# Optimization experiments

Hardware: AMD Instinct MI355X
Metric: run time of the kernel (lower is better)

## Reference

```python
import jax, jax.numpy as jnp
import numpy as np
import math

B, M, V, C, HID, BIN, H, W = 2, 1024, 300, 128, 128, 256, 384, 512


def fibonacci_sphere(n):
    # generate_grasp_views: n approximately-uniform directions on the unit sphere
    i = np.arange(n, dtype=np.float64)
    phi = (np.sqrt(5.0) - 1.0) / 2.0
    z = (2.0 * i + 1.0) / n - 1.0
    r = np.sqrt(np.maximum(1.0 - z * z, 0.0))
    t = 2.0 * np.pi * i * phi
    v = np.stack([r * np.cos(t), r * np.sin(t), z], -1)
    return (v / np.linalg.norm(v, axis=-1, keepdims=True)).astype(np.float32)


def setup_inputs():
    key = jax.random.key(0)
    ks = jax.random.split(key, 24)
    seed_features = jax.random.normal(ks[0], (B, C, M), jnp.float32)
    token_sel_idx = jax.random.randint(ks[1], (B, M), 0, H * W)
    fx = 525.0
    Kmat = jnp.array([[fx, 0.0, W / 2.0], [0.0, fx, H / 2.0], [0.0, 0.0, 1.0]], jnp.float32)
    K = jnp.broadcast_to(Kmat, (B, 3, 3))
    depth_map = 0.2 + 0.8 * jax.random.uniform(ks[2], (B, 1, H, W), jnp.float32)
    depth_prob = jax.nn.softmax(jax.random.normal(ks[3], (B, BIN, H, W), jnp.float32), axis=1)
    view_dirs = jnp.asarray(fibonacci_sphere(V))

    def lin(k, fan_in, shape):
        s = 1.0 / np.sqrt(fan_in)
        return jax.random.uniform(k, shape, jnp.float32, -s, s)

    qin = C + 7  # seed_feat + ray(3) + normal(3) + uncert(1)
    params = dict(
        Wq1=lin(ks[4], qin, (qin, HID)), bq1=lin(ks[5], qin, (HID,)),
        Wq2=lin(ks[6], HID, (HID, HID)), bq2=lin(ks[7], HID, (HID,)),
        Wa1=lin(ks[8], 3, (3, HID)), ba1=lin(ks[9], 3, (HID,)),
        Wa2=lin(ks[10], HID, (HID, HID)), ba2=lin(ks[11], HID, (HID,)),
        Wb1=lin(ks[12], 3, (3, HID // 2)), bb1=lin(ks[13], 3, (HID // 2,)),
        Wb2=lin(ks[14], HID // 2, (HID // 2, 1)), bb2=lin(ks[15], HID // 2, (1,)),
        Wr1=lin(ks[16], HID, (HID, C)), br1=lin(ks[17], HID, (C,)),
        Wr2=lin(ks[18], C, (C, C)), br2=lin(ks[19], C, (C,)),
    )
    return dict(seed_features=seed_features, token_sel_idx=token_sel_idx, K=K,
                depth_map=depth_map, depth_prob=depth_prob, view_dirs=view_dirs, **params)


def _views_to_rot(views):
    # batch_viewpoint_params_to_matrix(-views, angle=0)
    axis_x = -views
    zero = jnp.zeros_like(axis_x[..., 0])
    axis_y = jnp.stack([-axis_x[..., 1], axis_x[..., 0], zero], -1)
    ny = jnp.linalg.norm(axis_y, axis=-1, keepdims=True)
    fallback = jnp.broadcast_to(jnp.array([0.0, 1.0, 0.0], views.dtype), axis_y.shape)
    axis_y = jnp.where(ny < 1e-8, fallback, axis_y / jnp.maximum(ny, 1e-8))
    axis_x = axis_x / jnp.maximum(jnp.linalg.norm(axis_x, axis=-1, keepdims=True), 1e-8)
    axis_z = jnp.cross(axis_x, axis_y)
    return jnp.stack([axis_x, axis_y, axis_z], -1)  # (B,M,3,3)


def _forward(seed_features, token_sel_idx, K, depth_map, depth_prob, view_dirs,
             Wq1, bq1, Wq2, bq2, Wa1, ba1, Wa2, ba2, Wb1, bb1, Wb2, bb2, Wr1, br1, Wr2, br2):
    depth_map = jax.lax.stop_gradient(depth_map)   # .detach() in torch
    depth_prob = jax.lax.stop_gradient(depth_prob)
    # --- backproject depth to xyz map (B,3,H,W) ---
    ys, xs = jnp.meshgrid(jnp.arange(H, dtype=jnp.float32), jnp.arange(W, dtype=jnp.float32), indexing='ij')
    fx = K[:, 0, 0][:, None, None, None]; fy = K[:, 1, 1][:, None, None, None]
    cx = K[:, 0, 2][:, None, None, None]; cy = K[:, 1, 2][:, None, None, None]
    z = depth_map
    x = (xs[None, None] - cx) / fx * z
    y = (ys[None, None] - cy) / fy * z
    xyz = jnp.concatenate([x, y, z], axis=1)
    # --- central-difference normal map with replicate pad ---
    dx = (xyz[:, :, :, 2:] - xyz[:, :, :, :-2])[:, :, 1:-1, :]
    dy = (xyz[:, :, 2:, :] - xyz[:, :, :-2, :])[:, :, :, 1:-1]
    n = jnp.cross(dx.transpose(0, 2, 3, 1), dy.transpose(0, 2, 3, 1))
    n = n / jnp.maximum(jnp.linalg.norm(n, axis=-1, keepdims=True), 1e-6)
    normal_map = jnp.pad(n.transpose(0, 3, 1, 2), ((0, 0), (0, 0), (1, 1), (1, 1)), mode='edge')
    # --- depth uncertainty: normalized entropy over bins ---
    p = jnp.maximum(depth_prob, 1e-8)
    uncert_map = jnp.clip(-(p * jnp.log(p)).sum(axis=1, keepdims=True) / math.log(BIN), 0.0, 1.0)
    # --- per-seed irregular gathers ---
    def gather(feat, idx):
        Bf, Cf = feat.shape[0], feat.shape[1]
        flat = feat.reshape(Bf, Cf, H * W)
        return jnp.take_along_axis(flat, jnp.broadcast_to(idx[:, None, :], (Bf, Cf, idx.shape[1])), axis=2)
    normal_bm3 = gather(normal_map, token_sel_idx).transpose(0, 2, 1)  # (B,M,3)
    uncert_bm1 = gather(uncert_map, token_sel_idx).transpose(0, 2, 1)  # (B,M,1)
    u = (token_sel_idx % W).astype(jnp.float32)
    v = (token_sel_idx // W).astype(jnp.float32)
    rx = (u - K[:, 0, 2][:, None]) / K[:, 0, 0][:, None]
    ry = (v - K[:, 1, 2][:, None]) / K[:, 1, 1][:, None]
    rays = jnp.stack([rx, ry, jnp.ones_like(rx)], -1)
    rays = rays / jnp.maximum(jnp.linalg.norm(rays, axis=-1, keepdims=True), 1e-12)
    normal_bm3 = normal_bm3 * (1.0 - uncert_bm1)
    # --- query / anchor / bias MLPs ---
    q_in = jnp.concatenate([seed_features.transpose(0, 2, 1), rays, normal_bm3, uncert_bm1], -1)
    q = jax.nn.relu(jax.nn.relu(q_in @ Wq1 + bq1) @ Wq2 + bq2)          # (B,M,HID)
    a = jax.nn.relu(view_dirs @ Wa1 + ba1) @ Wa2 + ba2                  # (V,HID)
    bias = (jax.nn.relu(view_dirs @ Wb1 + bb1) @ Wb2 + bb2)[:, 0]        # (V,)
    logits = jnp.einsum('bmh,vh->bmv', q, a) / jnp.sqrt(jnp.float32(HID)) + bias
    view_score = jax.nn.sigmoid(logits)                                  # (B,M,V)
    # --- top-1 view selection + gather xyz / rot / anchor feat ---
    top_inds = jnp.argmax(view_score, axis=-1)                           # (B,M)
    top_xyz = view_dirs[top_inds]                                        # (B,M,3)
    rot = _views_to_rot(top_xyz)                                         # (B,M,3,3)
    top_a = a[top_inds]                                                  # (B,M,HID)
    res = jax.nn.relu((q + top_a) @ Wr1 + br1) @ Wr2 + br2               # (B,M,C)
    res_feat = res.transpose(0, 2, 1)                                    # (B,C,M)
    return view_score, top_inds, top_xyz, rot, res_feat


def reference(seed_features, token_sel_idx, K, depth_map, depth_prob, view_dirs,
              Wq1, bq1, Wq2, bq2, Wa1, ba1, Wa2, ba2, Wb1, bb1, Wb2, bb2, Wr1, br1, Wr2, br2):
    return _forward(seed_features, token_sel_idx, K, depth_map, depth_prob, view_dirs,
                    Wq1, bq1, Wq2, bq2, Wa1, ba1, Wa2, ba2, Wb1, bb1, Wb2, bb2, Wr1, br1, Wr2, br2)
```

## Files before the change

kernel.cpp:

```cpp
#include <hip/hip_runtime.h>
#include <math.h>

#define B 2
#define M 1024
#define V 300
#define C 128
#define HID 128
#define BIN 256
#define H 384
#define W 512
#define QIN (C + 7)
#define G 4

__global__ __launch_bounds__(HID) void anchor_kernel(
    const float* __restrict__ view_dirs,
    const float* __restrict__ Wa1, const float* __restrict__ ba1,
    const float* __restrict__ Wa2, const float* __restrict__ ba2,
    const float* __restrict__ Wb1, const float* __restrict__ bb1,
    const float* __restrict__ Wb2, const float* __restrict__ bb2,
    float* __restrict__ a_out, float* __restrict__ aT_out,
    float* __restrict__ bias_out) {
  const int v = blockIdx.x;
  const int t = threadIdx.x;
  __shared__ float h1[HID];

  const float vd0 = view_dirs[v * 3 + 0];
  const float vd1 = view_dirs[v * 3 + 1];
  const float vd2 = view_dirs[v * 3 + 2];

  float h = vd0 * Wa1[0 * HID + t] + vd1 * Wa1[1 * HID + t] + vd2 * Wa1[2 * HID + t] + ba1[t];
  h1[t] = fmaxf(h, 0.0f);

  if (t < 64) {
    float x = vd0 * Wb1[0 * 64 + t] + vd1 * Wb1[1 * 64 + t] + vd2 * Wb1[2 * 64 + t] + bb1[t];
    x = fmaxf(x, 0.0f) * Wb2[t];
#pragma unroll
    for (int o = 32; o > 0; o >>= 1) x += __shfl_down(x, o, 64);
    if (t == 0) bias_out[v] = x + bb2[0];
  }
  __syncthreads();

  float acc = ba2[t];
#pragma unroll 8
  for (int k = 0; k < HID; ++k) acc += h1[k] * Wa2[k * HID + t];
  a_out[v * HID + t] = acc;
  aT_out[(size_t)t * V + v] = acc;
}

__global__ __launch_bounds__(128) void seed_kernel(
    const float* __restrict__ seed, const int* __restrict__ token_sel_idx,
    const float* __restrict__ Kmat, const float* __restrict__ depth_map,
    const float* __restrict__ depth_prob, const float* __restrict__ view_dirs,
    const float* __restrict__ Wq1, const float* __restrict__ bq1,
    const float* __restrict__ Wq2, const float* __restrict__ bq2,
    const float* __restrict__ Wr1, const float* __restrict__ br1,
    const float* __restrict__ Wr2, const float* __restrict__ br2,
    const float* __restrict__ a_ws, const float* __restrict__ aT_ws,
    const float* __restrict__ bias_ws,
    float* __restrict__ out_view_score, float* __restrict__ out_top_inds,
    float* __restrict__ out_top_xyz, float* __restrict__ out_rot,
    float* __restrict__ out_res) {
  const int s0 = blockIdx.x * G;
  const int b = s0 >> 10;
  const int m0 = s0 & (M - 1);
  const int t = threadIdx.x;
  const int lane = t & 63;
  const int wv = t >> 6;

  __shared__ __align__(16) float qin_s[G][136];
  __shared__ __align__(16) float hs[G][HID];
  __shared__ __align__(16) float qs[G][HID];
  __shared__ __align__(16) float sum_s[G][HID];
  __shared__ float ered[G][2];
  __shared__ float wbv[G][2];
  __shared__ int   wbi[G][2];
  __shared__ int   sbest[G];
  __shared__ int   sidx[G];

  if (t < G) sidx[t] = token_sel_idx[b * M + m0 + t];

  {
    const float4 sv = *(const float4*)&seed[((size_t)b * C + t) * M + m0];
    qin_s[0][t] = sv.x; qin_s[1][t] = sv.y; qin_s[2][t] = sv.z; qin_s[3][t] = sv.w;
  }
  if (t < G) qin_s[t][135] = 0.0f;
  __syncthreads();

  {
    const size_t HW = (size_t)H * W;
    float e[G];
#pragma unroll
    for (int g = 0; g < G; ++g) {
      const float* dp = depth_prob + (size_t)b * BIN * HW + sidx[g];
      const float p0 = fmaxf(dp[(size_t)(2 * t + 0) * HW], 1e-8f);
      const float p1 = fmaxf(dp[(size_t)(2 * t + 1) * HW], 1e-8f);
      e[g] = p0 * logf(p0) + p1 * logf(p1);
    }
#pragma unroll
    for (int o = 32; o > 0; o >>= 1) {
#pragma unroll
      for (int g = 0; g < G; ++g) e[g] += __shfl_down(e[g], o, 64);
    }
    if (lane == 0) {
#pragma unroll
      for (int g = 0; g < G; ++g) ered[g][wv] = e[g];
    }
  }
  __syncthreads();

  if (t < G) {
    const int g = t;
    const int idx = sidx[g];
    float uncert = (-(ered[g][0] + ered[g][1])) / 5.5451774444795623f;
    uncert = fminf(fmaxf(uncert, 0.0f), 1.0f);

    const float fx = Kmat[b * 9 + 0], fy = Kmat[b * 9 + 4];
    const float cx = Kmat[b * 9 + 2], cy = Kmat[b * 9 + 5];
    const int w = idx % W;
    const int h = idx / W;
    const int hc = min(max(h, 1), H - 2);
    const int wc = min(max(w, 1), W - 2);

    const float* dm = depth_map + (size_t)b * H * W;
    const float zl = dm[hc * W + (wc - 1)];
    const float zr = dm[hc * W + (wc + 1)];
    const float zu = dm[(hc - 1) * W + wc];
    const float zd = dm[(hc + 1) * W + wc];

    const float dxx = (wc + 1 - cx) / fx * zr - (wc - 1 - cx) / fx * zl;
    const float dxy = (hc - cy) / fy * zr - (hc - cy) / fy * zl;
    const float dxz = zr - zl;
    const float dyx = (wc - cx) / fx * zd - (wc - cx) / fx * zu;
    const float dyy = (hc + 1 - cy) / fy * zd - (hc - 1 - cy) / fy * zu;
    const float dyz = zd - zu;

    float nx = dxy * dyz - dxz * dyy;
    float ny = dxz * dyx - dxx * dyz;
    float nz = dxx * dyy - dxy * dyx;
    const float nn = fmaxf(sqrtf(nx * nx + ny * ny + nz * nz), 1e-6f);
    const float sc = (1.0f - uncert) / nn;

    const float rx = ((float)w - cx) / fx;
    const float ry = ((float)h - cy) / fy;
    const float rn = fmaxf(sqrtf(rx * rx + ry * ry + 1.0f), 1e-12f);

    qin_s[g][128] = rx / rn;
    qin_s[g][129] = ry / rn;
    qin_s[g][130] = 1.0f / rn;
    qin_s[g][131] = nx * sc;
    qin_s[g][132] = ny * sc;
    qin_s[g][133] = nz * sc;
    qin_s[g][134] = uncert;
  }
  __syncthreads();

  {
    float acc[G];
    const float b1 = bq1[t];
#pragma unroll
    for (int g = 0; g < G; ++g) acc[g] = b1;
    for (int i0 = 0; i0 < 132; i0 += 4) {
      const float w0 = Wq1[(i0 + 0) * HID + t];
      const float w1 = Wq1[(i0 + 1) * HID + t];
      const float w2 = Wq1[(i0 + 2) * HID + t];
      const float w3 = Wq1[(i0 + 3) * HID + t];
#pragma unroll
      for (int g = 0; g < G; ++g) {
        const float4 qv = *(const float4*)&qin_s[g][i0];
        acc[g] += qv.x * w0 + qv.y * w1 + qv.z * w2 + qv.w * w3;
      }
    }
    {
      const float w0 = Wq1[132 * HID + t];
      const float w1 = Wq1[133 * HID + t];
      const float w2 = Wq1[134 * HID + t];
#pragma unroll
      for (int g = 0; g < G; ++g) {
        const float4 qv = *(const float4*)&qin_s[g][132];
        acc[g] += qv.x * w0 + qv.y * w1 + qv.z * w2;
      }
    }
#pragma unroll
    for (int g = 0; g < G; ++g) hs[g][t] = fmaxf(acc[g], 0.0f);
  }
  __syncthreads();

  {
    float acc[G];
    const float b2 = bq2[t];
#pragma unroll
    for (int g = 0; g < G; ++g) acc[g] = b2;
    for (int k0 = 0; k0 < HID; k0 += 4) {
      const float w0 = Wq2[(k0 + 0) * HID + t];
      const float w1 = Wq2[(k0 + 1) * HID + t];
      const float w2 = Wq2[(k0 + 2) * HID + t];
      const float w3 = Wq2[(k0 + 3) * HID + t];
#pragma unroll
      for (int g = 0; g < G; ++g) {
        const float4 hv = *(const float4*)&hs[g][k0];
        acc[g] += hv.x * w0 + hv.y * w1 + hv.z * w2 + hv.w * w3;
      }
    }
#pragma unroll
    for (int g = 0; g < G; ++g) qs[g][t] = fmaxf(acc[g], 0.0f);
  }
  __syncthreads();

  const int col2 = 256 + (t < 44 ? t : 43);
  float d0[G], d1[G], d2[G];
#pragma unroll
  for (int g = 0; g < G; ++g) { d0[g] = 0.0f; d1[g] = 0.0f; d2[g] = 0.0f; }
  for (int k0 = 0; k0 < HID; k0 += 4) {
    const float* r0 = aT_ws + (size_t)(k0 + 0) * V;
    const float* r1 = aT_ws + (size_t)(k0 + 1) * V;
    const float* r2 = aT_ws + (size_t)(k0 + 2) * V;
    const float* r3 = aT_ws + (size_t)(k0 + 3) * V;
    const float a00 = r0[t], a01 = r0[t + 128], a02 = r0[col2];
    const float a10 = r1[t], a11 = r1[t + 128], a12 = r1[col2];
    const float a20 = r2[t], a21 = r2[t + 128], a22 = r2[col2];
    const float a30 = r3[t], a31 = r3[t + 128], a32 = r3[col2];
#pragma unroll
    for (int g = 0; g < G; ++g) {
      const float4 qv = *(const float4*)&qs[g][k0];
      d0[g] += qv.x * a00 + qv.y * a10 + qv.z * a20 + qv.w * a30;
      d1[g] += qv.x * a01 + qv.y * a11 + qv.z * a21 + qv.w * a31;
      d2[g] += qv.x * a02 + qv.y * a12 + qv.z * a22 + qv.w * a32;
    }
  }

  const float rsq = 0.08838834764831845f;
  const float bw0 = bias_ws[t];
  const float bw1 = bias_ws[t + 128];
  const float bw2 = bias_ws[col2];
  float bv[G]; int bi[G];
#pragma unroll
  for (int g = 0; g < G; ++g) {
    const float sc0 = 1.0f / (1.0f + expf(-(d0[g] * rsq + bw0)));
    const float sc1 = 1.0f / (1.0f + expf(-(d1[g] * rsq + bw1)));
    const float sc2 = 1.0f / (1.0f + expf(-(d2[g] * rsq + bw2)));

    float* vs_out = out_view_score + (size_t)(b * M + m0 + g) * V;
    vs_out[t] = sc0;
    vs_out[t + 128] = sc1;
    if (t < 44) vs_out[t + 256] = sc2;

    bv[g] = sc0; bi[g] = t;
    if (sc1 > bv[g]) { bv[g] = sc1; bi[g] = t + 128; }
    if (t < 44 && sc2 > bv[g]) { bv[g] = sc2; bi[g] = t + 256; }
  }
#pragma unroll
  for (int o = 32; o > 0; o >>= 1) {
#pragma unroll
    for (int g = 0; g < G; ++g) {
      const float ov = __shfl_down(bv[g], o, 64);
      const int oi = __shfl_down(bi[g], o, 64);
      if (ov > bv[g] || (ov == bv[g] && oi < bi[g])) { bv[g] = ov; bi[g] = oi; }
    }
  }
  if (lane == 0) {
#pragma unroll
    for (int g = 0; g < G; ++g) { wbv[g][wv] = bv[g]; wbi[g][wv] = bi[g]; }
  }
  __syncthreads();

  if (t < G) {
    const int g = t;
    float fbv = wbv[g][0]; int fbi = wbi[g][0];
    if (wbv[g][1] > fbv || (wbv[g][1] == fbv && wbi[g][1] < fbi)) { fbv = wbv[g][1]; fbi = wbi[g][1]; }
    sbest[g] = fbi;

    const int bm = b * M + m0 + g;
    out_top_inds[bm] = (float)fbi;
    const float vx = view_dirs[fbi * 3 + 0];
    const float vy = view_dirs[fbi * 3 + 1];
    const float vz = view_dirs[fbi * 3 + 2];
    out_top_xyz[(size_t)bm * 3 + 0] = vx;
    out_top_xyz[(size_t)bm * 3 + 1] = vy;
    out_top_xyz[(size_t)bm * 3 + 2] = vz;

    float ax0 = -vx, ax1 = -vy, ax2 = -vz;
    float ay0 = vy, ay1 = -vx, ay2 = 0.0f;
    const float nyn = sqrtf(ay0 * ay0 + ay1 * ay1);
    if (nyn < 1e-8f) {
      ay0 = 0.0f; ay1 = 1.0f; ay2 = 0.0f;
    } else {
      const float d = fmaxf(nyn, 1e-8f);
      ay0 /= d; ay1 /= d;
    }
    const float an = fmaxf(sqrtf(ax0 * ax0 + ax1 * ax1 + ax2 * ax2), 1e-8f);
    ax0 /= an; ax1 /= an; ax2 /= an;
    const float az0 = ax1 * ay2 - ax2 * ay1;
    const float az1 = ax2 * ay0 - ax0 * ay2;
    const float az2 = ax0 * ay1 - ax1 * ay0;
    float* R = out_rot + (size_t)bm * 9;
    R[0] = ax0; R[1] = ay0; R[2] = az0;
    R[3] = ax1; R[4] = ay1; R[5] = az1;
    R[6] = ax2; R[7] = ay2; R[8] = az2;
  }
  __syncthreads();

#pragma unroll
  for (int g = 0; g < G; ++g) sum_s[g][t] = qs[g][t] + a_ws[sbest[g] * HID + t];
  __syncthreads();

  {
    float acc[G];
    const float b1 = br1[t];
#pragma unroll
    for (int g = 0; g < G; ++g) acc[g] = b1;
    for (int k0 = 0; k0 < HID; k0 += 4) {
      const float w0 = Wr1[(k0 + 0) * HID + t];
      const float w1 = Wr1[(k0 + 1) * HID + t];
      const float w2 = Wr1[(k0 + 2) * HID + t];
      const float w3 = Wr1[(k0 + 3) * HID + t];
#pragma unroll
      for (int g = 0; g < G; ++g) {
        const float4 sv = *(const float4*)&sum_s[g][k0];
        acc[g] += sv.x * w0 + sv.y * w1 + sv.z * w2 + sv.w * w3;
      }
    }
#pragma unroll
    for (int g = 0; g < G; ++g) hs[g][t] = fmaxf(acc[g], 0.0f);
  }
  __syncthreads();

  {
    float acc[G];
    const float b2 = br2[t];
#pragma unroll
    for (int g = 0; g < G; ++g) acc[g] = b2;
    for (int k0 = 0; k0 < HID; k0 += 4) {
      const float w0 = Wr2[(k0 + 0) * HID + t];
      const float w1 = Wr2[(k0 + 1) * HID + t];
      const float w2 = Wr2[(k0 + 2) * HID + t];
      const float w3 = Wr2[(k0 + 3) * HID + t];
#pragma unroll
      for (int g = 0; g < G; ++g) {
        const float4 hv = *(const float4*)&hs[g][k0];
        acc[g] += hv.x * w0 + hv.y * w1 + hv.z * w2 + hv.w * w3;
      }
    }
    float4 o;
    o.x = acc[0]; o.y = acc[1]; o.z = acc[2]; o.w = acc[3];
    *(float4*)&out_res[((size_t)b * C + t) * M + m0] = o;
  }
}

extern "C" void kernel_launch(void* const* d_in, const int* in_sizes, int n_in,
                              void* d_out, int out_size, void* d_ws, size_t ws_size,
                              hipStream_t stream) {
  const float* seed  = (const float*)d_in[0];
  const int*   tok   = (const int*)d_in[1];
  const float* Km    = (const float*)d_in[2];
  const float* dmap  = (const float*)d_in[3];
  const float* dprob = (const float*)d_in[4];
  const float* vdirs = (const float*)d_in[5];
  const float* Wq1 = (const float*)d_in[6];  const float* bq1 = (const float*)d_in[7];
  const float* Wq2 = (const float*)d_in[8];  const float* bq2 = (const float*)d_in[9];
  const float* Wa1 = (const float*)d_in[10]; const float* ba1 = (const float*)d_in[11];
  const float* Wa2 = (const float*)d_in[12]; const float* ba2 = (const float*)d_in[13];
  const float* Wb1 = (const float*)d_in[14]; const float* bb1 = (const float*)d_in[15];
  const float* Wb2 = (const float*)d_in[16]; const float* bb2 = (const float*)d_in[17];
  const float* Wr1 = (const float*)d_in[18]; const float* br1 = (const float*)d_in[19];
  const float* Wr2 = (const float*)d_in[20]; const float* br2 = (const float*)d_in[21];

  float* out = (float*)d_out;
  float* vs  = out;
  float* ti  = vs + (size_t)B * M * V;
  float* tx  = ti + (size_t)B * M;
  float* rot = tx + (size_t)B * M * 3;
  float* rf  = rot + (size_t)B * M * 9;

  float* a_ws    = (float*)d_ws;
  float* aT_ws   = a_ws + (size_t)V * HID;
  float* bias_ws = aT_ws + (size_t)HID * V;

  anchor_kernel<<<V, HID, 0, stream>>>(vdirs, Wa1, ba1, Wa2, ba2, Wb1, bb1, Wb2, bb2,
                                       a_ws, aT_ws, bias_ws);
  seed_kernel<<<(B * M) / G, 128, 0, stream>>>(seed, tok, Km, dmap, dprob, vdirs,
                                               Wq1, bq1, Wq2, bq2, Wr1, br1, Wr2, br2,
                                               a_ws, aT_ws, bias_ws, vs, ti, tx, rot, rf);
}
```

Before: 544.6 us.

## Overlap depth-prob and depth-map gathers with the seed-feature part of the first MLP layer

The kernel now issues the scattered depth_prob loads and the per-token depth_map neighbour loads early, holding them in registers. It then runs the 128 seed-feature rows of the Wq1 matvec before computing the entropy and normals, so the gather latency is hidden behind that arithmetic. The last 7 geometry inputs are added in a separate small loop once uncertainty and normals are ready. Register pressure goes up from the 8 buffered probabilities plus the depth and index values.

New measurement: 548.1 us. Within noise of the previous version (+0.6%).

```diff
diff --git a/kernel.cpp b/kernel.cpp
--- a/kernel.cpp
+++ b/kernel.cpp
@@ -79,21 +79,63 @@
 
   if (t < G) sidx[t] = token_sel_idx[b * M + m0 + t];
 
-  {
-    const float4 sv = *(const float4*)&seed[((size_t)b * C + t) * M + m0];
-    qin_s[0][t] = sv.x; qin_s[1][t] = sv.y; qin_s[2][t] = sv.z; qin_s[3][t] = sv.w;
-  }
-  if (t < G) qin_s[t][135] = 0.0f;
-  __syncthreads();
-
+  const float4 sv = *(const float4*)&seed[((size_t)b * C + t) * M + m0];
+  __syncthreads();
+
+  float pe[2 * G];
   {
     const size_t HW = (size_t)H * W;
-    float e[G];
 #pragma unroll
     for (int g = 0; g < G; ++g) {
       const float* dp = depth_prob + (size_t)b * BIN * HW + sidx[g];
-      const float p0 = fmaxf(dp[(size_t)(2 * t + 0) * HW], 1e-8f);
-      const float p1 = fmaxf(dp[(size_t)(2 * t + 1) * HW], 1e-8f);
+      pe[2 * g + 0] = dp[(size_t)(2 * t + 0) * HW];
+      pe[2 * g + 1] = dp[(size_t)(2 * t + 1) * HW];
+    }
+  }
+
+  float zl = 0.f, zr = 0.f, zu = 0.f, zd = 0.f;
+  int w_r = 0, h_r = 0, wc_r = 0, hc_r = 0;
+  if (t < G) {
+    const int idx = sidx[t];
+    w_r = idx % W;
+    h_r = idx / W;
+    hc_r = min(max(h_r, 1), H - 2);
+    wc_r = min(max(w_r, 1), W - 2);
+    const float* dm = depth_map + (size_t)b * H * W;
+    zl = dm[hc_r * W + (wc_r - 1)];
+    zr = dm[hc_r * W + (wc_r + 1)];
+    zu = dm[(hc_r - 1) * W + wc_r];
+    zd = dm[(hc_r + 1) * W + wc_r];
+  }
+
+  qin_s[0][t] = sv.x; qin_s[1][t] = sv.y; qin_s[2][t] = sv.z; qin_s[3][t] = sv.w;
+  if (t < G) qin_s[t][135] = 0.0f;
+  __syncthreads();
+
+  float acc[G];
+  {
+    const float b1 = bq1[t];
+#pragma unroll
+    for (int g = 0; g < G; ++g) acc[g] = b1;
+    for (int i0 = 0; i0 < 128; i0 += 4) {
+      const float w0 = Wq1[(i0 + 0) * HID + t];
+      const float w1 = Wq1[(i0 + 1) * HID + t];
+      const float w2 = Wq1[(i0 + 2) * HID + t];
+      const float w3 = Wq1[(i0 + 3) * HID + t];
+#pragma unroll
+      for (int g = 0; g < G; ++g) {
+        const float4 qv = *(const float4*)&qin_s[g][i0];
+        acc[g] += qv.x * w0 + qv.y * w1 + qv.z * w2 + qv.w * w3;
+      }
+    }
+  }
+
+  {
+    float e[G];
+#pragma unroll
+    for (int g = 0; g < G; ++g) {
+      const float p0 = fmaxf(pe[2 * g + 0], 1e-8f);
+      const float p1 = fmaxf(pe[2 * g + 1], 1e-8f);
       e[g] = p0 * logf(p0) + p1 * logf(p1);
     }
 #pragma unroll
@@ -110,22 +152,12 @@
 
   if (t < G) {
     const int g = t;
-    const int idx = sidx[g];
     float uncert = (-(ered[g][0] + ered[g][1])) / 5.5451774444795623f;
     uncert = fminf(fmaxf(uncert, 0.0f), 1.0f);
 
     const float fx = Kmat[b * 9 + 0], fy = Kmat[b * 9 + 4];
     const float cx = Kmat[b * 9 + 2], cy = Kmat[b * 9 + 5];
-    const int w = idx % W;
-    const int h = idx / W;
-    const int hc = min(max(h, 1), H - 2);
-    const int wc = min(max(w, 1), W - 2);
-
-    const float* dm = depth_map + (size_t)b * H * W;
-    const float zl = dm[hc * W + (wc - 1)];
-    const float zr = dm[hc * W + (wc + 1)];
-    const float zu = dm[(hc - 1) * W + wc];
-    const float zd = dm[(hc + 1) * W + wc];
+    const int w = w_r, h = h_r, hc = hc_r, wc = wc_r;
 
     const float dxx = (wc + 1 - cx) / fx * zr - (wc - 1 - cx) / fx * zl;
     const float dxy = (hc - cy) / fy * zr - (hc - cy) / fy * zl;
@@ -155,30 +187,11 @@
   __syncthreads();
 
   {
-    float acc[G];
-    const float b1 = bq1[t];
-#pragma unroll
-    for (int g = 0; g < G; ++g) acc[g] = b1;
-    for (int i0 = 0; i0 < 132; i0 += 4) {
-      const float w0 = Wq1[(i0 + 0) * HID + t];
-      const float w1 = Wq1[(i0 + 1) * HID + t];
-      const float w2 = Wq1[(i0 + 2) * HID + t];
-      const float w3 = Wq1[(i0 + 3) * HID + t];
-#pragma unroll
-      for (int g = 0; g < G; ++g) {
-        const float4 qv = *(const float4*)&qin_s[g][i0];
-        acc[g] += qv.x * w0 + qv.y * w1 + qv.z * w2 + qv.w * w3;
-      }
-    }
-    {
-      const float w0 = Wq1[132 * HID + t];
-      const float w1 = Wq1[133 * HID + t];
-      const float w2 = Wq1[134 * HID + t];
-#pragma unroll
-      for (int g = 0; g < G; ++g) {
-        const float4 qv = *(const float4*)&qin_s[g][132];
-        acc[g] += qv.x * w0 + qv.y * w1 + qv.z * w2;
-      }
+#pragma unroll
+    for (int i = 128; i < 135; ++i) {
+      const float wv_ = Wq1[i * HID + t];
+#pragma unroll
+      for (int g = 0; g < G; ++g) acc[g] += qin_s[g][i] * wv_;
     }
 #pragma unroll
     for (int g = 0; g < G; ++g) hs[g][t] = fmaxf(acc[g], 0.0f);
@@ -186,7 +199,6 @@
   __syncthreads();
 
   {
-    float acc[G];
     const float b2 = bq2[t];
 #pragma unroll
     for (int g = 0; g < G; ++g) acc[g] = b2;
@@ -304,7 +316,6 @@
   __syncthreads();
 
   {
-    float acc[G];
     const float b1 = br1[t];
 #pragma unroll
     for (int g = 0; g < G; ++g) acc[g] = b1;
@@ -315,8 +326,8 @@
       const float w3 = Wr1[(k0 + 3) * HID + t];
 #pragma unroll
       for (int g = 0; g < G; ++g) {
-        const float4 sv = *(const float4*)&sum_s[g][k0];
-        acc[g] += sv.x * w0 + sv.y * w1 + sv.z * w2 + sv.w * w3;
+        const float4 sv2 = *(const float4*)&sum_s[g][k0];
+        acc[g] += sv2.x * w0 + sv2.y * w1 + sv2.z * w2 + sv2.w * w3;
       }
     }
 #pragma unroll
@@ -325,7 +336,6 @@
   __syncthreads();
 
   {
-    float acc[G];
     const float b2 = br2[t];
 #pragma unroll
     for (int g = 0; g < G; ++g) acc[g] = b2;
```
